# Optimization experiments

Hardware: AMD Instinct MI355X
Metric: run time of the kernel (lower is better)

Reference implementation:

```python
import jax, jax.numpy as jnp
import numpy as np

N_NODES = 50000
N_EDGES = 800000
D_IN = 128
D_OUT = 128


def setup_inputs() -> dict:
    key = jax.random.key(0)
    k1, k2, k3, k4, k5 = jax.random.split(key, 5)
    feature = jax.random.normal(k1, (N_NODES, D_IN), dtype=jnp.float32)
    src = jax.random.randint(k2, (N_EDGES,), 0, N_NODES, dtype=jnp.int32)
    dst = jax.random.randint(k3, (N_EDGES,), 0, N_NODES, dtype=jnp.int32)
    # nn.Linear default init scale ~ 1/sqrt(in_feats)
    W = jax.random.normal(k4, (D_OUT, D_IN), dtype=jnp.float32) / np.sqrt(D_IN)
    b = jax.random.normal(k5, (D_OUT,), dtype=jnp.float32) / np.sqrt(D_IN)
    return {"feature": feature, "src": src, "dst": dst, "W": W, "b": b}


def reference(feature, src, dst, W, b):
    # update_all(copy_src, sum): gather source node features per edge,
    # scatter-add into destination nodes -> [N, D_IN]
    msgs = feature[src]  # [E, D_IN]
    agg = jax.ops.segment_sum(msgs, dst, num_segments=N_NODES)
    # apply_nodes: linear + activation
    z = jax.nn.relu(agg @ W.T + b)
    # residual: in_feats == out_feats -> identity down path
    return z + feature
```

## Files before the change

### kernel.cpp

```cpp
#include <hip/hip_runtime.h>

#define N_NODES 50000
#define N_EDGES 800000
#define D 128
#define NTILES 782
#define XCAP 16
#define CAP 64

typedef unsigned short ushort_t;
typedef unsigned int uint_t;
typedef __attribute__((ext_vector_type(8))) short bf16x8;
typedef __attribute__((ext_vector_type(4))) float f32x4;

#define WS_COUNTS8 0
#define WS_ESRC8   (8 * 50048)
#define WS_FB16    (WS_ESRC8 + 3200000)
#define WS_WB16    (WS_FB16 + N_NODES * D / 2)
#define WS_FULL_BYTES ((size_t)(WS_WB16 + D * D / 2) * 4)
#define WS_COUNTS 0
#define WS_ESRC   50048
#define WS_CSR_BYTES ((size_t)(WS_ESRC + N_NODES * CAP) * 4)

__device__ inline uint_t pack2bf16(float lo, float hi) {
  uint_t ulo = __builtin_bit_cast(uint_t, lo);
  uint_t uhi = __builtin_bit_cast(uint_t, hi);
  ulo = (ulo + 0x7fffu + ((ulo >> 16) & 1u)) >> 16;
  uhi = (uhi + 0x7fffu + ((uhi >> 16) & 1u)) & 0xffff0000u;
  return ulo | uhi;
}

__global__ __launch_bounds__(256) void prep_build_kernel(
    const float* __restrict__ f, const float* __restrict__ W,
    const int* __restrict__ src, const int* __restrict__ dst,
    int* __restrict__ counts8, ushort_t* __restrict__ esrc8,
    ushort_t* __restrict__ fb, ushort_t* __restrict__ wb) {
  const int i = blockIdx.x * 256 + threadIdx.x;
  {
    const float4 v0 = ((const float4*)f)[2 * i];
    const float4 v1 = ((const float4*)f)[2 * i + 1];
    uint_t r[4];
    r[0] = pack2bf16(v0.x, v0.y);
    r[1] = pack2bf16(v0.z, v0.w);
    r[2] = pack2bf16(v1.x, v1.y);
    r[3] = pack2bf16(v1.z, v1.w);
    *(uint4*)(fb + (size_t)i * 8) = *(const uint4*)r;
  }
  if (i < D * D / 8) {
    const float4 v0 = ((const float4*)W)[2 * i];
    const float4 v1 = ((const float4*)W)[2 * i + 1];
    uint_t r[4];
    r[0] = pack2bf16(v0.x, v0.y);
    r[1] = pack2bf16(v0.z, v0.w);
    r[2] = pack2bf16(v1.x, v1.y);
    r[3] = pack2bf16(v1.z, v1.w);
    *(uint4*)(wb + (size_t)i * 8) = *(const uint4*)r;
  }
  {
    const int s = src[i];
    const int d = dst[i];
    const int x = blockIdx.x & 7;
    const int pos = atomicAdd(&counts8[x * 50048 + d], 1);
    if (pos < XCAP)
      esrc8[(size_t)x * (N_NODES * XCAP) + d * XCAP + pos] = (ushort_t)s;
  }
}

__global__ __launch_bounds__(256) void gather_slice_kernel(
    const ushort_t* __restrict__ fb16,
    const int* __restrict__ counts8,
    const ushort_t* __restrict__ esrc8,
    float* __restrict__ agg) {
  const int x     = blockIdx.x & 7;
  const int j     = blockIdx.x >> 3;
  const int tile  = j * 2 + (x & 1);
  const int slice = x >> 1;
  const int row0  = tile * 64;
  const int l = threadIdx.x & 3;
  const int g = threadIdx.x >> 2;
  const int row = row0 + g;
  const int col0 = slice * 32 + l * 8;

  float a[8];
#pragma unroll
  for (int k = 0; k < 8; ++k) a[k] = 0.f;

  if (row < N_NODES) {
    int cn[8];
#pragma unroll
    for (int xx = 0; xx < 8; ++xx) {
      int c = counts8[xx * 50048 + row];
      cn[xx] = c > XCAP ? XCAP : c;
    }
#pragma unroll
    for (int xx = 0; xx < 8; ++xx) {
      const int cnt = cn[xx];
      const ushort_t* ep = esrc8 + (size_t)xx * (N_NODES * XCAP) + row * XCAP;
      for (int j0 = 0; j0 < cnt; j0 += 4) {
        int eid = 0;
        if (j0 + l < cnt) eid = ep[j0 + l];
        const int lim = (cnt - j0 < 4) ? (cnt - j0) : 4;
        for (int k = 0; k < lim; ++k) {
          const int s = __shfl(eid, k, 4);
          const uint4 w4 = *(const uint4*)(fb16 + (size_t)s * D + col0);
          const uint_t ws[4] = {w4.x, w4.y, w4.z, w4.w};
#pragma unroll
          for (int q = 0; q < 4; ++q) {
            a[2 * q]     += __builtin_bit_cast(float, ws[q] << 16);
            a[2 * q + 1] += __builtin_bit_cast(float, ws[q] & 0xffff0000u);
          }
        }
      }
    }
    float* p = agg + (size_t)row * D + col0;
    *(float4*)p       = make_float4(a[0], a[1], a[2], a[3]);
    *(float4*)(p + 4) = make_float4(a[4], a[5], a[6], a[7]);
  }
}

#define RPB 32
__global__ __launch_bounds__(256) void transform_mfma_kernel(
    float* __restrict__ agg_out,
    const float* __restrict__ feature,
    const ushort_t* __restrict__ wb16,
    const float* __restrict__ b) {
  __shared__ float sA[RPB][D + 4];

  const int tid  = threadIdx.x;
  const int row0 = blockIdx.x * RPB;

  for (int i = tid; i < RPB * (D / 4); i += 256) {
    const int r  = i >> 5;
    const int c4 = (i & 31) * 4;
    const int row = row0 + r;
    float4 v = make_float4(0.f, 0.f, 0.f, 0.f);
    if (row < N_NODES) v = *(const float4*)(agg_out + (size_t)row * D + c4);
    *(float4*)&sA[r][c4] = v;
  }
  __syncthreads();

  const int wave = tid >> 6;
  const int lane = tid & 63;
  const int lr = lane & 15;
  const int lk = lane >> 4;

  f32x4 acc00 = {0.f, 0.f, 0.f, 0.f}, acc01 = acc00;
  f32x4 acc10 = acc00, acc11 = acc00;

#pragma unroll
  for (int ks = 0; ks < 4; ++ks) {
    bf16x8 afr[2];
#pragma unroll
    for (int mt = 0; mt < 2; ++mt) {
      const float* ap = &sA[mt * 16 + lr][ks * 32 + lk * 8];
      const float4 a0 = *(const float4*)ap;
      const float4 a1 = *(const float4*)(ap + 4);
      uint_t u[4];
      u[0] = pack2bf16(a0.x, a0.y);
      u[1] = pack2bf16(a0.z, a0.w);
      u[2] = pack2bf16(a1.x, a1.y);
      u[3] = pack2bf16(a1.z, a1.w);
      afr[mt] = __builtin_bit_cast(bf16x8, *(const uint4*)u);
    }
    bf16x8 bfr[2];
#pragma unroll
    for (int ntl = 0; ntl < 2; ++ntl) {
      const int col = (2 * wave + ntl) * 16 + lr;
      bfr[ntl] = *(const bf16x8*)(wb16 + (size_t)col * D + ks * 32 + lk * 8);
    }
    acc00 = __builtin_amdgcn_mfma_f32_16x16x32_bf16(afr[0], bfr[0], acc00, 0, 0, 0);
    acc01 = __builtin_amdgcn_mfma_f32_16x16x32_bf16(afr[0], bfr[1], acc01, 0, 0, 0);
    acc10 = __builtin_amdgcn_mfma_f32_16x16x32_bf16(afr[1], bfr[0], acc10, 0, 0, 0);
    acc11 = __builtin_amdgcn_mfma_f32_16x16x32_bf16(afr[1], bfr[1], acc11, 0, 0, 0);
  }

#pragma unroll
  for (int mt = 0; mt < 2; ++mt) {
#pragma unroll
    for (int ntl = 0; ntl < 2; ++ntl) {
      const f32x4 av = (mt == 0) ? (ntl == 0 ? acc00 : acc01)
                                 : (ntl == 0 ? acc10 : acc11);
      const int col = (2 * wave + ntl) * 16 + lr;
      const float bias = b[col];
#pragma unroll
      for (int jj = 0; jj < 4; ++jj) {
        const int row = row0 + mt * 16 + lk * 4 + jj;
        if (row < N_NODES) {
          const size_t o = (size_t)row * D + col;
          float z = av[jj] + bias;
          z = z > 0.f ? z : 0.f;
          agg_out[o] = z + feature[o];
        }
      }
    }
  }
}

__global__ __launch_bounds__(256) void build_kernel(const int* __restrict__ src,
                                                    const int* __restrict__ dst,
                                                    int* __restrict__ counts,
                                                    int* __restrict__ esrc) {
  const int e = blockIdx.x * 256 + threadIdx.x;
  if (e < N_EDGES) {
    const int d = dst[e];
    const int pos = atomicAdd(&counts[d], 1);
    if (pos < CAP) esrc[(size_t)d * CAP + pos] = src[e];
  }
}

__global__ __launch_bounds__(256) void gather_transform_f32_kernel(
    const float* __restrict__ feature,
    const int* __restrict__ counts,
    const int* __restrict__ esrc,
    const float* __restrict__ W,
    const float* __restrict__ b,
    float* __restrict__ out) {
  __shared__ float sA[RPB][D];
  const int tid  = threadIdx.x;
  const int row0 = blockIdx.x * RPB;
  const int l = tid & 15;
  const int g = tid >> 4;
#pragma unroll
  for (int p = 0; p < 2; ++p) {
    const int r   = p * 16 + g;
    const int row = row0 + r;
    float4 a0 = make_float4(0.f, 0.f, 0.f, 0.f);
    float4 a1 = make_float4(0.f, 0.f, 0.f, 0.f);
    if (row < N_NODES) {
      int cnt = counts[row];
      if (cnt > CAP) cnt = CAP;
      const size_t base = (size_t)row * CAP;
      for (int j0 = 0; j0 < cnt; j0 += 16) {
        int eid = 0;
        if (j0 + l < cnt) eid = esrc[base + j0 + l];
        const int lim = (cnt - j0 < 16) ? (cnt - j0) : 16;
        for (int k = 0; k < lim; ++k) {
          const int s = __shfl(eid, k, 16);
          const float* fp = feature + (size_t)s * D + l * 8;
          const float4 v0 = *(const float4*)fp;
          const float4 v1 = *(const float4*)(fp + 4);
          a0.x += v0.x; a0.y += v0.y; a0.z += v0.z; a0.w += v0.w;
          a1.x += v1.x; a1.y += v1.y; a1.z += v1.z; a1.w += v1.w;
        }
      }
    }
    float4* sp = (float4*)&sA[r][l * 8];
    sp[0] = a0; sp[1] = a1;
  }
  __syncthreads();
  const int c  = tid & 127;
  const int rh = tid >> 7;
  float acc[16];
#pragma unroll
  for (int r = 0; r < 16; ++r) acc[r] = 0.f;
  for (int k = 0; k < D; ++k) {
    const float wv = W[c * D + k];
#pragma unroll
    for (int r = 0; r < 16; ++r) acc[r] += sA[rh * 16 + r][k] * wv;
  }
  const float bias = b[c];
#pragma unroll
  for (int r = 0; r < 16; ++r) {
    const int row = row0 + rh * 16 + r;
    if (row < N_NODES) {
      const size_t o = (size_t)row * D + c;
      float z = acc[r] + bias;
      z = z > 0.f ? z : 0.f;
      out[o] = z + feature[o];
    }
  }
}

__global__ __launch_bounds__(256) void scatter_kernel(
    const float* __restrict__ feature,
    const int* __restrict__ src,
    const int* __restrict__ dst,
    float* __restrict__ agg) {
  const long long total = (long long)N_EDGES * (D / 4);
  long long idx = (long long)blockIdx.x * blockDim.x + threadIdx.x;
  const long long stride = (long long)gridDim.x * blockDim.x;
  for (; idx < total; idx += stride) {
    const int e  = (int)(idx >> 5);
    const int c4 = ((int)idx & 31) * 4;
    const float4 v = *(const float4*)(feature + (long long)src[e] * D + c4);
    float* p = agg + (long long)dst[e] * D + c4;
    atomicAdd(p + 0, v.x);
    atomicAdd(p + 1, v.y);
    atomicAdd(p + 2, v.z);
    atomicAdd(p + 3, v.w);
  }
}

__global__ __launch_bounds__(256) void transform_kernel(
    float* __restrict__ agg_out,
    const float* __restrict__ feature,
    const float* __restrict__ W,
    const float* __restrict__ b) {
  __shared__ float sA[RPB][D];
  const int row0 = blockIdx.x * RPB;
  for (int i = threadIdx.x; i < RPB * (D / 4); i += 256) {
    const int r  = i >> 5;
    const int c4 = (i & 31) * 4;
    const int row = row0 + r;
    float4 v = make_float4(0.f, 0.f, 0.f, 0.f);
    if (row < N_NODES) v = *(const float4*)(agg_out + (long long)row * D + c4);
    *(float4*)&sA[r][c4] = v;
  }
  __syncthreads();
  const int c  = threadIdx.x & 127;
  const int rh = threadIdx.x >> 7;
  float acc[16];
#pragma unroll
  for (int r = 0; r < 16; ++r) acc[r] = 0.f;
  for (int k = 0; k < D; ++k) {
    const float wv = W[c * D + k];
#pragma unroll
    for (int r = 0; r < 16; ++r) acc[r] += sA[rh * 16 + r][k] * wv;
  }
  const float bias = b[c];
#pragma unroll
  for (int r = 0; r < 16; ++r) {
    const int row = row0 + rh * 16 + r;
    if (row < N_NODES) {
      const long long o = (long long)row * D + c;
      float z = acc[r] + bias;
      z = z > 0.f ? z : 0.f;
      agg_out[o] = z + feature[o];
    }
  }
}

extern "C" void kernel_launch(void* const* d_in, const int* in_sizes, int n_in,
                              void* d_out, int out_size, void* d_ws, size_t ws_size,
                              hipStream_t stream) {
  const float* feature = (const float*)d_in[0];
  const int*   src     = (const int*)d_in[1];
  const int*   dst     = (const int*)d_in[2];
  const float* W       = (const float*)d_in[3];
  const float* b       = (const float*)d_in[4];
  float* out = (float*)d_out;

  const int eblocks = (N_EDGES + 255) / 256;
  const int nblocks = (N_NODES + RPB - 1) / RPB;

  if (ws_size >= WS_FULL_BYTES) {
    int*      wsi     = (int*)d_ws;
    int*      counts8 = wsi + WS_COUNTS8;
    ushort_t* esrc8   = (ushort_t*)(wsi + WS_ESRC8);
    ushort_t* fb16    = (ushort_t*)(wsi + WS_FB16);
    ushort_t* wb16    = (ushort_t*)(wsi + WS_WB16);

    hipMemsetAsync(counts8, 0, (size_t)8 * 50048 * 4, stream);
    prep_build_kernel<<<eblocks, 256, 0, stream>>>(feature, W, src, dst,
                                                   counts8, esrc8, fb16, wb16);
    const int gje = (NTILES + 1) / 2;
    gather_slice_kernel<<<gje * 8, 256, 0, stream>>>(fb16, counts8, esrc8, out);
    transform_mfma_kernel<<<nblocks, 256, 0, stream>>>(out, feature, wb16, b);
  } else if (ws_size >= WS_CSR_BYTES) {
    int* wsi    = (int*)d_ws;
    int* counts = wsi + WS_COUNTS;
    int* esrc   = wsi + WS_ESRC;

    hipMemsetAsync(counts, 0, (size_t)N_NODES * 4, stream);
    build_kernel<<<eblocks, 256, 0, stream>>>(src, dst, counts, esrc);
    gather_transform_f32_kernel<<<nblocks, 256, 0, stream>>>(feature, counts,
                                                             esrc, W, b, out);
  } else {
    hipMemsetAsync(out, 0, (size_t)N_NODES * D * sizeof(float), stream);
    scatter_kernel<<<2048, 256, 0, stream>>>(feature, src, dst, out);
    transform_kernel<<<nblocks, 256, 0, stream>>>(out, feature, W, b);
  }
}
```

Before: 192.9 us.

## Fuse memset, build, gather and MFMA transform into one cooperative kernel

```diff
diff --git a/kernel.cpp b/kernel.cpp
--- a/kernel.cpp
+++ b/kernel.cpp
@@ -1,4 +1,7 @@
 #include <hip/hip_runtime.h>
+#include <hip/hip_cooperative_groups.h>
+
+namespace cg = cooperative_groups;
 
 #define N_NODES 50000
 #define N_EDGES 800000
@@ -6,6 +9,8 @@
 #define NTILES 782
 #define XCAP 16
 #define CAP 64
+#define COOP_BLOCKS 1024
+#define GUNITS (391 * 8)
 
 typedef unsigned short ushort_t;
 typedef unsigned int uint_t;
@@ -27,6 +32,180 @@
   ulo = (ulo + 0x7fffu + ((ulo >> 16) & 1u)) >> 16;
   uhi = (uhi + 0x7fffu + ((uhi >> 16) & 1u)) & 0xffff0000u;
   return ulo | uhi;
+}
+
+__global__ __launch_bounds__(256, 4) void fused_kernel(
+    const float* __restrict__ feature, const float* __restrict__ W,
+    const int* __restrict__ src, const int* __restrict__ dst,
+    int* __restrict__ counts8, ushort_t* __restrict__ esrc8,
+    ushort_t* __restrict__ fb16, ushort_t* __restrict__ wb16,
+    const float* __restrict__ b, float* __restrict__ out) {
+  __shared__ float sA[32][D + 4];
+
+  cg::grid_group grid = cg::this_grid();
+  const int tid   = threadIdx.x;
+  const int bid   = blockIdx.x;
+  const int gsz   = gridDim.x * 256;
+  const int gidx0 = bid * 256 + tid;
+
+  for (int i = gidx0; i < 8 * 50048; i += gsz) counts8[i] = 0;
+  grid.sync();
+
+  {
+    const int x = bid & 7;
+    for (int i = gidx0; i < N_EDGES; i += gsz) {
+      {
+        const float4 v0 = ((const float4*)feature)[2 * i];
+        const float4 v1 = ((const float4*)feature)[2 * i + 1];
+        uint_t r[4];
+        r[0] = pack2bf16(v0.x, v0.y);
+        r[1] = pack2bf16(v0.z, v0.w);
+        r[2] = pack2bf16(v1.x, v1.y);
+        r[3] = pack2bf16(v1.z, v1.w);
+        *(uint4*)(fb16 + (size_t)i * 8) = *(const uint4*)r;
+      }
+      if (i < D * D / 8) {
+        const float4 v0 = ((const float4*)W)[2 * i];
+        const float4 v1 = ((const float4*)W)[2 * i + 1];
+        uint_t r[4];
+        r[0] = pack2bf16(v0.x, v0.y);
+        r[1] = pack2bf16(v0.z, v0.w);
+        r[2] = pack2bf16(v1.x, v1.y);
+        r[3] = pack2bf16(v1.z, v1.w);
+        *(uint4*)(wb16 + (size_t)i * 8) = *(const uint4*)r;
+      }
+      {
+        const int s = src[i];
+        const int d = dst[i];
+        const int pos = atomicAdd(&counts8[x * 50048 + d], 1);
+        if (pos < XCAP)
+          esrc8[(size_t)x * (N_NODES * XCAP) + d * XCAP + pos] = (ushort_t)s;
+      }
+    }
+  }
+  grid.sync();
+
+  {
+    const int l = tid & 3;
+    const int g = tid >> 2;
+    for (int u = bid; u < GUNITS; u += COOP_BLOCKS) {
+      const int x     = u & 7;
+      const int j     = u >> 3;
+      const int tile  = j * 2 + (x & 1);
+      const int slice = x >> 1;
+      const int row   = tile * 64 + g;
+      const int col0  = slice * 32 + l * 8;
+      if (row >= N_NODES) continue;
+
+      float a[8];
+#pragma unroll
+      for (int k = 0; k < 8; ++k) a[k] = 0.f;
+
+      int cn[8];
+#pragma unroll
+      for (int xx = 0; xx < 8; ++xx) {
+        int c = counts8[xx * 50048 + row];
+        cn[xx] = c > XCAP ? XCAP : c;
+      }
+#pragma unroll
+      for (int xx = 0; xx < 8; ++xx) {
+        const int cnt = cn[xx];
+        const ushort_t* ep = esrc8 + (size_t)xx * (N_NODES * XCAP) + row * XCAP;
+        for (int j0 = 0; j0 < cnt; j0 += 4) {
+          int eid = 0;
+          if (j0 + l < cnt) eid = ep[j0 + l];
+          const int lim = (cnt - j0 < 4) ? (cnt - j0) : 4;
+          for (int k = 0; k < lim; ++k) {
+            const int s = __shfl(eid, k, 4);
+            const uint4 w4 = *(const uint4*)(fb16 + (size_t)s * D + col0);
+            const uint_t ws[4] = {w4.x, w4.y, w4.z, w4.w};
+#pragma unroll
+            for (int q = 0; q < 4; ++q) {
+              a[2 * q]     += __builtin_bit_cast(float, ws[q] << 16);
+              a[2 * q + 1] += __builtin_bit_cast(float, ws[q] & 0xffff0000u);
+            }
+          }
+        }
+      }
+      float* p = out + (size_t)row * D + col0;
+      *(float4*)p       = make_float4(a[0], a[1], a[2], a[3]);
+      *(float4*)(p + 4) = make_float4(a[4], a[5], a[6], a[7]);
+    }
+  }
+  grid.sync();
+
+  {
+    const int wave = tid >> 6;
+    const int lane = tid & 63;
+    const int lr = lane & 15;
+    const int lk = lane >> 4;
+    const int ntiles = (N_NODES + 31) / 32;
+
+    for (int t = bid; t < ntiles; t += COOP_BLOCKS) {
+      const int row0 = t * 32;
+      __syncthreads();
+      for (int i = tid; i < 32 * (D / 4); i += 256) {
+        const int r  = i >> 5;
+        const int c4 = (i & 31) * 4;
+        const int row = row0 + r;
+        float4 v = make_float4(0.f, 0.f, 0.f, 0.f);
+        if (row < N_NODES) v = *(const float4*)(out + (size_t)row * D + c4);
+        *(float4*)&sA[r][c4] = v;
+      }
+      __syncthreads();
+
+      f32x4 acc00 = {0.f, 0.f, 0.f, 0.f}, acc01 = acc00;
+      f32x4 acc10 = acc00, acc11 = acc00;
+
+#pragma unroll
+      for (int ks = 0; ks < 4; ++ks) {
+        bf16x8 afr[2];
+#pragma unroll
+        for (int mt = 0; mt < 2; ++mt) {
+          const float* ap = &sA[mt * 16 + lr][ks * 32 + lk * 8];
+          const float4 a0 = *(const float4*)ap;
+          const float4 a1 = *(const float4*)(ap + 4);
+          uint_t u4[4];
+          u4[0] = pack2bf16(a0.x, a0.y);
+          u4[1] = pack2bf16(a0.z, a0.w);
+          u4[2] = pack2bf16(a1.x, a1.y);
+          u4[3] = pack2bf16(a1.z, a1.w);
+          afr[mt] = __builtin_bit_cast(bf16x8, *(const uint4*)u4);
+        }
+        bf16x8 bfr[2];
+#pragma unroll
+        for (int ntl = 0; ntl < 2; ++ntl) {
+          const int col = (2 * wave + ntl) * 16 + lr;
+          bfr[ntl] = *(const bf16x8*)(wb16 + (size_t)col * D + ks * 32 + lk * 8);
+        }
+        acc00 = __builtin_amdgcn_mfma_f32_16x16x32_bf16(afr[0], bfr[0], acc00, 0, 0, 0);
+        acc01 = __builtin_amdgcn_mfma_f32_16x16x32_bf16(afr[0], bfr[1], acc01, 0, 0, 0);
+        acc10 = __builtin_amdgcn_mfma_f32_16x16x32_bf16(afr[1], bfr[0], acc10, 0, 0, 0);
+        acc11 = __builtin_amdgcn_mfma_f32_16x16x32_bf16(afr[1], bfr[1], acc11, 0, 0, 0);
+      }
+
+#pragma unroll
+      for (int mt = 0; mt < 2; ++mt) {
+#pragma unroll
+        for (int ntl = 0; ntl < 2; ++ntl) {
+          const f32x4 av = (mt == 0) ? (ntl == 0 ? acc00 : acc01)
+                                     : (ntl == 0 ? acc10 : acc11);
+          const int col = (2 * wave + ntl) * 16 + lr;
+          const float bias = b[col];
+#pragma unroll
+          for (int jj = 0; jj < 4; ++jj) {
+            const int row = row0 + mt * 16 + lk * 4 + jj;
+            if (row < N_NODES) {
+              const size_t o = (size_t)row * D + col;
+              float z = av[jj] + bias;
+              z = z > 0.f ? z : 0.f;
+              out[o] = z + feature[o];
+            }
+          }
+        }
+      }
+    }
+  }
 }
 
 __global__ __launch_bounds__(256) void prep_build_kernel(
@@ -349,6 +528,13 @@
     ushort_t* fb16    = (ushort_t*)(wsi + WS_FB16);
     ushort_t* wb16    = (ushort_t*)(wsi + WS_WB16);
 
+    void* args[] = {(void*)&feature, (void*)&W, (void*)&src, (void*)&dst,
+                    (void*)&counts8, (void*)&esrc8, (void*)&fb16, (void*)&wb16,
+                    (void*)&b, (void*)&out};
+    hipError_t err = hipLaunchCooperativeKernel(
+        (const void*)fused_kernel, dim3(COOP_BLOCKS), dim3(256), args, 0, stream);
+    if (err == hipSuccess) return;
+
     hipMemsetAsync(counts8, 0, (size_t)8 * 50048 * 4, stream);
     prep_build_kernel<<<eblocks, 256, 0, stream>>>(feature, W, src, dst,
                                                    counts8, esrc8, fb16, wb16);
```

After: 549.2 us. 2.85x slower.
